# Kernel tuning notes

Hardware: AMD Instinct MI355X
Metric: run time of the kernel (lower is better)

The kernel has to match this reference:

```python
import jax, jax.numpy as jnp
import numpy as np

# Static config matching init_kwargs / input_specs
B, C, H, W, T = 2, 128, 32, 32, 32
OUT = 256
WS, SHIFT, HEADS = 4, 2, 8
MLP = 4 * C
N = WS ** 3          # tokens per 4x4x4 window = 64
D_BLOCKS = 4         # depth=2 -> 2 (no-shift, shift) pairs


def _rel_idx():
    coords = np.stack(np.meshgrid(np.arange(WS), np.arange(WS), np.arange(WS), indexing='ij')).reshape(3, -1)
    rel = (coords[:, :, None] - coords[:, None, :]).transpose(1, 2, 0) + (WS - 1)
    return (rel[..., 0] * (2 * WS - 1) ** 2 + rel[..., 1] * (2 * WS - 1) + rel[..., 2]).astype(np.int32)

REL_IDX = jnp.asarray(_rel_idx())  # [N, N]


def _attn_mask():
    # Faithful port of Block.createmask (H,W,T already multiples of WS)
    img = np.zeros((H, W, T))
    sl = (slice(0, -WS), slice(-WS, -SHIFT), slice(-SHIFT, None))
    cnt = 0
    for hs in sl:
        for ws_ in sl:
            for ts in sl:
                img[hs, ws_, ts] = cnt
                cnt += 1
    m = img.reshape(H // WS, WS, W // WS, WS, T // WS, WS).transpose(0, 2, 4, 1, 3, 5).reshape(-1, N)
    am = m[:, None, :] - m[:, :, None]
    return jnp.asarray(np.where(am != 0, -100.0, 0.0).astype(np.float32))  # [nW, N, N]

MASK = _attn_mask()


def _partition(x):  # [b,H,W,T,c] -> [b*nW, N, c]
    b, c = x.shape[0], x.shape[-1]
    x = x.reshape(b, H // WS, WS, W // WS, WS, T // WS, WS, c).transpose(0, 1, 3, 5, 2, 4, 6, 7)
    return x.reshape(-1, N, c)


def _reverse(wins, b, c):  # [b*nW, N, c] -> [b,H,W,T,c]
    x = wins.reshape(b, H // WS, W // WS, T // WS, WS, WS, WS, c).transpose(0, 1, 4, 2, 5, 3, 6, 7)
    return x.reshape(b, H, W, T, c)


def _ln(x, g, b):
    mu = x.mean(-1, keepdims=True)
    var = ((x - mu) ** 2).mean(-1, keepdims=True)
    return (x - mu) / jnp.sqrt(var + 1e-5) * g + b


def _swin(x, shift, g1, b1, qw, qb, pw, pb, rpb, g2, b2, f1w, f1b, f2w, f2b):
    b, L, c = x.shape
    hd = c // HEADS
    scale = hd ** -0.5
    h = _ln(x, g1, b1).reshape(b, H, W, T, c)
    if shift:
        h = jnp.roll(h, (-SHIFT, -SHIFT, -SHIFT), axis=(1, 2, 3))
    win = _partition(h)  # [b*nW, N, c]
    qkv = (win @ qw.T + qb).reshape(-1, N, 3, HEADS, hd).transpose(2, 0, 3, 1, 4)
    q, k, v = qkv[0] * scale, qkv[1], qkv[2]
    attn = jnp.einsum('bhnd,bhmd->bhnm', q, k) + rpb[REL_IDX].transpose(2, 0, 1)[None]
    if shift:
        nW = MASK.shape[0]
        attn = (attn.reshape(b, nW, HEADS, N, N) + MASK[None, :, None]).reshape(-1, HEADS, N, N)
    attn = jax.nn.softmax(attn, axis=-1)
    o = jnp.einsum('bhnm,bhmd->bhnd', attn, v).transpose(0, 2, 1, 3).reshape(-1, N, c)
    o = o @ pw.T + pb
    h = _reverse(o, b, c)
    if shift:
        h = jnp.roll(h, (SHIFT, SHIFT, SHIFT), axis=(1, 2, 3))
    x = x + h.reshape(b, L, c)
    m = jax.nn.gelu(_ln(x, g2, b2) @ f1w.T + f1b, approximate=False)
    return x + (m @ f2w.T + f2b)


def setup_inputs() -> dict:
    key = jax.random.key(0)
    ks = jax.random.split(key, 10)
    r = lambda i, sh, s=0.02: jax.random.normal(ks[i], sh, jnp.float32) * s
    Dn = D_BLOCKS
    return {
        'x': jax.random.normal(ks[0], (B, C, H, W, T), jnp.float32),
        'norm1_g': jnp.ones((Dn, C), jnp.float32), 'norm1_b': jnp.zeros((Dn, C), jnp.float32),
        'qkv_w': r(1, (Dn, 3 * C, C)), 'qkv_b': jnp.zeros((Dn, 3 * C), jnp.float32),
        'proj_w': r(2, (Dn, C, C)), 'proj_b': jnp.zeros((Dn, C), jnp.float32),
        'rpb': r(3, (Dn, (2 * WS - 1) ** 3, HEADS)),
        'norm2_g': jnp.ones((Dn, C), jnp.float32), 'norm2_b': jnp.zeros((Dn, C), jnp.float32),
        'fc1_w': r(4, (Dn, MLP, C)), 'fc1_b': jnp.zeros((Dn, MLP), jnp.float32),
        'fc2_w': r(5, (Dn, C, MLP)), 'fc2_b': jnp.zeros((Dn, C), jnp.float32),
        'dw_w': r(6, (C, 1, 3, 3, 3), 0.1), 'dw_b': jnp.zeros((C,), jnp.float32),
        'pw_w': r(7, (OUT, C, 1, 1, 1), 0.05), 'pw_b': jnp.zeros((OUT,), jnp.float32),
        'bn_g': jnp.ones((OUT,), jnp.float32), 'bn_b': jnp.zeros((OUT,), jnp.float32),
    }


def reference(x, norm1_g, norm1_b, qkv_w, qkv_b, proj_w, proj_b, rpb, norm2_g, norm2_b,
              fc1_w, fc1_b, fc2_w, fc2_b, dw_w, dw_b, pw_w, pw_b, bn_g, bn_b):
    b = x.shape[0]
    t = x.transpose(0, 2, 3, 4, 1).reshape(b, H * W * T, C)  # b (h w t) c
    shifts = [0, SHIFT, 0, SHIFT]
    for i, s in enumerate(shifts):
        t = _swin(t, s, norm1_g[i], norm1_b[i], qkv_w[i], qkv_b[i], proj_w[i], proj_b[i],
                  rpb[i], norm2_g[i], norm2_b[i], fc1_w[i], fc1_b[i], fc2_w[i], fc2_b[i])
    y = t.reshape(b, H, W, T, C).transpose(0, 4, 1, 2, 3)
    # connectBlock: depthwise 3x3x3 conv + pointwise 1x1x1 conv + BatchNorm3d + ReLU
    dn = ('NCDHW', 'OIDHW', 'NCDHW')
    y = jax.lax.conv_general_dilated(y, dw_w, (1, 1, 1), 'SAME', dimension_numbers=dn,
                                     feature_group_count=C) + dw_b[None, :, None, None, None]
    y = jax.lax.conv_general_dilated(y, pw_w, (1, 1, 1), 'SAME', dimension_numbers=dn) + pw_b[None, :, None, None, None]
    mu = y.mean((0, 2, 3, 4), keepdims=True)
    var = ((y - mu) ** 2).mean((0, 2, 3, 4), keepdims=True)
    y = (y - mu) / jnp.sqrt(var + 1e-5) * bn_g[None, :, None, None, None] + bn_b[None, :, None, None, None]
    return jax.nn.relu(y)
```

## Files before the change

kernel.cpp:

```cpp
#include <hip/hip_runtime.h>
#include <hip/hip_bf16.h>
#include <cstddef>
#include <cstdint>

typedef __attribute__((ext_vector_type(8))) short short8;
typedef __attribute__((ext_vector_type(4))) short short4v;
typedef __attribute__((ext_vector_type(4))) float floatx4;
typedef __hip_bfloat16 bf16;

#define HEADS 8
#define TOK   65536
#define OUTC  256

__device__ inline float b2f(short s) {
    union { unsigned u; float f; } x;
    x.u = ((unsigned)(unsigned short)s) << 16;
    return x.f;
}

__device__ inline floatx4 mfma16(short4v a, short4v b, floatx4 c) {
#if __has_builtin(__builtin_amdgcn_mfma_f32_16x16x16bf16_1k)
    return __builtin_amdgcn_mfma_f32_16x16x16bf16_1k(a, b, c, 0, 0, 0);
#else
    floatx4 d;
    asm volatile("v_mfma_f32_16x16x16_bf16 %0, %1, %2, %3\n\ts_nop 7"
                 : "=v"(d) : "v"(a), "v"(b), "v"(c));
    return d;
#endif
}

__global__ __launch_bounds__(256) void transpose_in_kernel(
    const float* __restrict__ x, float* __restrict__ out, float* __restrict__ tstats)
{
    __shared__ float tile[128 * 65];
    int chunk = blockIdx.x;
    int tid = threadIdx.x;
    int b = chunk >> 9;
    int sp0 = (chunk & 511) * 64;
    #pragma unroll
    for (int l = 0; l < 32; ++l) {
        int idx = l * 256 + tid;
        int c = idx >> 6;
        int s = idx & 63;
        tile[c * 65 + s] = x[(((size_t)(b * 128 + c)) << 15) + sp0 + s];
    }
    __syncthreads();
    #pragma unroll
    for (int l = 0; l < 32; ++l) {
        int idx = l * 256 + tid;
        int s = idx >> 7;
        int c = idx & 127;
        out[((size_t)((b << 15) + sp0 + s)) * 128 + c] = tile[c * 65 + s];
    }
    int s = tid >> 2, q = tid & 3;
    float sm = 0.f, sq = 0.f;
    #pragma unroll
    for (int cc = 0; cc < 32; ++cc) {
        float v = tile[(q * 32 + cc) * 65 + s];
        sm += v; sq += v * v;
    }
    sm += __shfl_xor(sm, 1); sq += __shfl_xor(sq, 1);
    sm += __shfl_xor(sm, 2); sq += __shfl_xor(sq, 2);
    if (q == 0) {
        float mu = sm * (1.0f / 128.0f);
        float var = sq * (1.0f / 128.0f) - mu * mu;
        size_t tok = (size_t)(b << 15) + sp0 + s;
        tstats[tok * 2]     = mu;
        tstats[tok * 2 + 1] = rsqrtf(var + 1e-5f);
    }
}

__global__ __launch_bounds__(256) void prep_kernel(
    const float* __restrict__ qkv_w, const float* __restrict__ proj_w,
    const float* __restrict__ fc1_w, const float* __restrict__ fc2_w,
    const float* __restrict__ pw_w, const float* __restrict__ dw_w,
    bf16* __restrict__ wbf, float* __restrict__ dwt, float* __restrict__ stats)
{
    int i = blockIdx.x * 256 + threadIdx.x;
    float v;
    if (i < 196608)       v = qkv_w[i];
    else if (i < 262144)  v = proj_w[i - 196608];
    else if (i < 524288)  v = fc1_w[i - 262144];
    else if (i < 786432)  v = fc2_w[i - 524288];
    else                  v = pw_w[i - 786432];
    wbf[i] = __float2bfloat16(v);
    if (i < 3456) {
        int c = i / 27, k = i % 27;
        dwt[k * 128 + c] = dw_w[i];
    }
    if (i < 512) stats[i] = 0.f;
}

__global__ __launch_bounds__(256) void pack_kernel(
    const float* __restrict__ fc1_w, const float* __restrict__ fc2_w,
    bf16* __restrict__ pw1, bf16* __restrict__ pw2)
{
    int t = blockIdx.x * 256 + threadIdx.x;
    int i = t >> 17;
    int rem = t & 131071;
    int type = rem >> 16;
    int idx = rem & 65535;
    int j = idx & 7, lane = (idx >> 3) & 63;
    int ln15 = lane & 15, quad = lane >> 4;
    if (type == 0) {
        int nt = (idx >> 9) & 1, kk = (idx >> 10) & 3, wv = (idx >> 12) & 3, cc = (idx >> 14) & 3;
        int row = cc * 128 + wv * 32 + nt * 16 + ln15;
        int col = kk * 32 + quad * 8 + j;
        pw1[i * 65536 + idx] = __float2bfloat16(fc1_w[(size_t)i * 65536 + row * 128 + col]);
    } else {
        int nt = (idx >> 9) & 1, ks = (idx >> 10) & 3, cc = (idx >> 12) & 3, wv = (idx >> 14) & 3;
        int row = wv * 32 + nt * 16 + ln15;
        int col = cc * 128 + ks * 32 + quad * 8 + j;
        pw2[i * 65536 + idx] = __float2bfloat16(fc2_w[(size_t)i * 65536 + row * 512 + col]);
    }
}

__global__ __launch_bounds__(256) void rpe_expand_kernel(
    const float* __restrict__ rpb, float* __restrict__ rpe, int layer)
{
    int t = blockIdx.x * 256 + threadIdx.x;
    int j = t & 63, i = (t >> 6) & 63, head = (t >> 12) & 7, wt = t >> 15;
    int ih = i >> 4, iw = (i >> 2) & 3, it = i & 3;
    int jh = j >> 4, jw = (j >> 2) & 3, jt = j & 3;
    int ridx = ((ih - jh + 3) * 7 + (iw - jw + 3)) * 7 + (it - jt + 3);
    float v = rpb[layer * 2744 + ridx * 8 + head];
    if (wt) {
        bool ok = true;
        if (wt & 4) ok = ok && ((ih >= 2) == (jh >= 2));
        if (wt & 2) ok = ok && ((iw >= 2) == (jw >= 2));
        if (wt & 1) ok = ok && ((it >= 2) == (jt >= 2));
        if (!ok) v -= 100.f;
    }
    rpe[t] = v;
}

__global__ __launch_bounds__(256) void gemm_bf16_kernel(
    const bf16* __restrict__ A, const bf16* __restrict__ Bw,
    const float* __restrict__ bias, bf16* __restrict__ Cb, float* __restrict__ Cf,
    float* __restrict__ aux, const float* __restrict__ p1, const float* __restrict__ p2,
    int M, int N, int K, int mode, int shift)
{
    __shared__ __align__(16) char smem[34816];
    __shared__ float cs[128];
    __shared__ float cq[128];
    short* As = (short*)smem;
    short* Bs = (short*)(smem + 8192);
    int tid = threadIdx.x;
    int lane = tid & 63, wv = tid >> 6;
    int wm = wv >> 1, wn = wv & 1;
    int ln15 = lane & 15, quad = lane >> 4;
    int q8 = quad * 8;
    int nBase = blockIdx.x * 128;
    int mBase = blockIdx.y * 128;
    floatx4 acc[4][4] = {};

    if (mode == 4 && tid < 128) { cs[tid] = 0.f; cq[tid] = 0.f; }

    int srow = tid >> 2, scb = tid & 3;

    int toks[2]; float tmu[2], trs[2];
    if (mode == 0) {
        if (tid < 128) { cs[tid] = p1[tid]; cq[tid] = p2[tid]; }
        #pragma unroll
        for (int i = 0; i < 2; ++i) {
            int m = mBase + srow + i * 64;
            int n = m & 63, w = (m >> 6) & 511, b = m >> 15;
            int ih = n >> 4, iw = (n >> 2) & 3, it = n & 3;
            int wh = w >> 6, ww = (w >> 3) & 7, wt = w & 7;
            int h  = (wh * 4 + ih + shift) & 31;
            int w2 = (ww * 4 + iw + shift) & 31;
            int t  = (wt * 4 + it + shift) & 31;
            toks[i] = (b << 15) + ((h * 32 + w2) * 32 + t);
            tmu[i] = aux[(size_t)toks[i] * 2];
            trs[i] = aux[(size_t)toks[i] * 2 + 1];
        }
        __syncthreads();
    }

    for (int k0 = 0; k0 < K; k0 += 32) {
        if (mode == 0) {
            int cb = k0 + scb * 8;
            #pragma unroll
            for (int i = 0; i < 2; ++i) {
                const float* xr = Cf + (size_t)toks[i] * 128 + cb;
                float4 a0 = *(const float4*)xr;
                float4 a1 = *(const float4*)(xr + 4);
                float mu = tmu[i], rs = trs[i];
                __align__(16) bf16 pk[8];
                pk[0] = __float2bfloat16((a0.x - mu) * rs * cs[cb + 0] + cq[cb + 0]);
                pk[1] = __float2bfloat16((a0.y - mu) * rs * cs[cb + 1] + cq[cb + 1]);
                pk[2] = __float2bfloat16((a0.z - mu) * rs * cs[cb + 2] + cq[cb + 2]);
                pk[3] = __float2bfloat16((a0.w - mu) * rs * cs[cb + 3] + cq[cb + 3]);
                pk[4] = __float2bfloat16((a1.x - mu) * rs * cs[cb + 4] + cq[cb + 4]);
                pk[5] = __float2bfloat16((a1.y - mu) * rs * cs[cb + 5] + cq[cb + 5]);
                pk[6] = __float2bfloat16((a1.z - mu) * rs * cs[cb + 6] + cq[cb + 6]);
                pk[7] = __float2bfloat16((a1.w - mu) * rs * cs[cb + 7] + cq[cb + 7]);
                ((uint4*)As)[i * 256 + tid] = *(const uint4*)pk;
                ((uint4*)Bs)[i * 256 + tid] =
                    *(const uint4*)(Bw + (size_t)(nBase + srow + i * 64) * K + cb);
            }
        } else {
            #pragma unroll
            for (int i = 0; i < 2; ++i) {
                int row = srow + i * 64;
                ((uint4*)As)[i * 256 + tid] =
                    *(const uint4*)(A + (size_t)(mBase + row) * K + k0 + scb * 8);
                ((uint4*)Bs)[i * 256 + tid] =
                    *(const uint4*)(Bw + (size_t)(nBase + row) * K + k0 + scb * 8);
            }
        }
        __syncthreads();
        short8 af[4], bfr[4];
        #pragma unroll
        for (int mt = 0; mt < 4; ++mt)
            af[mt] = *(const short8*)&As[(wm * 64 + mt * 16 + ln15) * 32 + q8];
        #pragma unroll
        for (int nt = 0; nt < 4; ++nt)
            bfr[nt] = *(const short8*)&Bs[(wn * 64 + nt * 16 + ln15) * 32 + q8];
        #pragma unroll
        for (int mt = 0; mt < 4; ++mt)
            #pragma unroll
            for (int nt = 0; nt < 4; ++nt)
                acc[mt][nt] = __builtin_amdgcn_mfma_f32_16x16x32_bf16(
                    af[mt], bfr[nt], acc[mt][nt], 0, 0, 0);
        __syncthreads();
    }

    if (mode == 4) {
        #pragma unroll
        for (int nt = 0; nt < 4; ++nt) {
            int nl = wn * 64 + nt * 16 + ln15;
            float bs = bias[nBase + nl];
            float s = 0.f, sq = 0.f;
            #pragma unroll
            for (int mt = 0; mt < 4; ++mt)
                #pragma unroll
                for (int r = 0; r < 4; ++r) {
                    float v = acc[mt][nt][r] + bs;
                    s += v; sq += v * v;
                }
            atomicAdd(&cs[nl], s);
            atomicAdd(&cq[nl], sq);
        }
        __syncthreads();
        if (tid < 128) {
            atomicAdd(&aux[nBase + tid], cs[tid]);
            atomicAdd(&aux[256 + nBase + tid], cq[tid]);
        }
        return;
    }

    if (mode == 0) {
        bf16* estage = (bf16*)smem;
        float qsc = (nBase == 0) ? 0.25f : 1.0f;
        #pragma unroll
        for (int mt = 0; mt < 4; ++mt)
            #pragma unroll
            for (int nt = 0; nt < 4; ++nt)
                #pragma unroll
                for (int r = 0; r < 4; ++r) {
                    int row = wm * 64 + mt * 16 + quad * 4 + r;
                    int col = wn * 64 + nt * 16 + ln15;
                    estage[row * 136 + col] =
                        __float2bfloat16((acc[mt][nt][r] + bias[nBase + col]) * qsc);
                }
        __syncthreads();
        int row = tid >> 1, hf = tid & 1;
        #pragma unroll
        for (int j = 0; j < 4; ++j) {
            int col = hf * 64 + j * 16;
            *(uint4*)(Cb + (size_t)(mBase + row) * N + nBase + col) =
                *(const uint4*)&estage[row * 136 + col];
            *(uint4*)(Cb + (size_t)(mBase + row) * N + nBase + col + 8) =
                *(const uint4*)&estage[row * 136 + col + 8];
        }
        return;
    }

    if (mode == 2) {
        float* fstage = (float*)smem;
        #pragma unroll
        for (int hf = 0; hf < 2; ++hf) {
            if (wm == hf) {
                #pragma unroll
                for (int mt = 0; mt < 4; ++mt)
                    #pragma unroll
                    for (int nt = 0; nt < 4; ++nt)
                        #pragma unroll
                        for (int r = 0; r < 4; ++r) {
                            int ml = mt * 16 + quad * 4 + r;
                            int col = wn * 64 + nt * 16 + ln15;
                            fstage[ml * 132 + col] = acc[mt][nt][r] + bias[col];
                        }
            }
            __syncthreads();
            int tl = tid >> 2, part = tid & 3;
            int g = mBase + hf * 64 + tl;
            int n_ = g & 63, w = (g >> 6) & 511, b = g >> 15;
            int ih = n_ >> 4, iw = (n_ >> 2) & 3, it = n_ & 3;
            int wh = w >> 6, ww = (w >> 3) & 7, wt = w & 7;
            int h  = (wh * 4 + ih + shift) & 31;
            int w2 = (ww * 4 + iw + shift) & 31;
            int t  = (wt * 4 + it + shift) & 31;
            size_t tok = ((size_t)b << 15) + ((h * 32 + w2) * 32 + t);
            float* dst = aux + tok * 128 + part * 32;
            #pragma unroll
            for (int j = 0; j < 8; ++j) {
                float4 a = *(float4*)(dst + j * 4);
                float4 l = *(const float4*)&fstage[tl * 132 + part * 32 + j * 4];
                a.x += l.x; a.y += l.y; a.z += l.z; a.w += l.w;
                *(float4*)(dst + j * 4) = a;
            }
            __syncthreads();
        }
        return;
    }

    {
        float* fstage = (float*)smem;
        int b = mBase >> 15, sp0 = mBase & 32767;
        #pragma unroll
        for (int hf = 0; hf < 2; ++hf) {
            if (wn == hf) {
                #pragma unroll
                for (int nt = 0; nt < 4; ++nt) {
                    int ncol = nt * 16 + ln15;
                    int nn = nBase + hf * 64 + ncol;
                    float mean = aux[nn] * (1.0f / 65536.0f);
                    float var  = aux[256 + nn] * (1.0f / 65536.0f) - mean * mean;
                    float sc = rsqrtf(var + 1e-5f) * p1[nn];
                    float off = p2[nn] + bias[nn] * sc - mean * sc;
                    #pragma unroll
                    for (int mt = 0; mt < 4; ++mt)
                        #pragma unroll
                        for (int r = 0; r < 4; ++r) {
                            int ml = wm * 64 + mt * 16 + quad * 4 + r;
                            float y = acc[mt][nt][r] * sc + off;
                            fstage[ncol * 132 + ml] = fmaxf(y, 0.f);
                        }
                }
            }
            __syncthreads();
            int nl = tid >> 2, part = tid & 3;
            int nn = nBase + hf * 64 + nl;
            float* dst = Cf + (((size_t)(b * 256 + nn)) << 15) + sp0 + part * 32;
            #pragma unroll
            for (int j = 0; j < 8; ++j)
                *(float4*)(dst + j * 4) = *(const float4*)&fstage[nl * 132 + part * 32 + j * 4];
            __syncthreads();
        }
    }
}

__global__ __launch_bounds__(256, 4) void mlp_kernel(
    float* __restrict__ xbuf, const float* __restrict__ g, const float* __restrict__ bta,
    const bf16* __restrict__ pw1, const float* __restrict__ b1,
    const bf16* __restrict__ pw2, const float* __restrict__ b2,
    bf16* __restrict__ xout16, float* __restrict__ tstats)
{
    __shared__ __align__(16) bf16 smem[64 * 136 * 2];
    bf16* aln  = smem;
    bf16* hidc = smem + 64 * 136;
    float* ostage = (float*)smem;
    int tid = threadIdx.x;
    int lane = tid & 63, wv = tid >> 6;
    int ln15 = lane & 15, quad = lane >> 4;
    int q8 = quad * 8;
    size_t tok0 = (size_t)blockIdx.x * 64;

    #pragma unroll
    for (int itk = 0; itk < 16; ++itk) {
        int t = wv * 16 + itk;
        const float* xp = xbuf + (tok0 + t) * 128;
        float v0 = xp[lane], v1 = xp[lane + 64];
        float s = v0 + v1, sq = v0 * v0 + v1 * v1;
        #pragma unroll
        for (int o = 32; o > 0; o >>= 1) { s += __shfl_xor(s, o); sq += __shfl_xor(sq, o); }
        float mu  = s * (1.0f / 128.0f);
        float var = sq * (1.0f / 128.0f) - mu * mu;
        float rs  = rsqrtf(var + 1e-5f);
        aln[t * 136 + lane]      = __float2bfloat16((v0 - mu) * rs * g[lane]      + bta[lane]);
        aln[t * 136 + lane + 64] = __float2bfloat16((v1 - mu) * rs * g[lane + 64] + bta[lane + 64]);
    }
    __syncthreads();

    floatx4 acc2[4][2] = {};
    #pragma unroll
    for (int cc = 0; cc < 4; ++cc) {
        floatx4 acc[4][2] = {};
        const bf16* p1w = pw1 + (size_t)(cc * 4 + wv) * 4096;
        #pragma unroll
        for (int kk = 0; kk < 4; ++kk) {
            short8 af[4], bfr[2];
            #pragma unroll
            for (int mt = 0; mt < 4; ++mt)
                af[mt] = *(const short8*)&aln[(mt * 16 + ln15) * 136 + kk * 32 + q8];
            #pragma unroll
            for (int nt = 0; nt < 2; ++nt)
                bfr[nt] = *(const short8*)(p1w + kk * 1024 + nt * 512 + lane * 8);
            #pragma unroll
            for (int mt = 0; mt < 4; ++mt)
                #pragma unroll
                for (int nt = 0; nt < 2; ++nt)
                    acc[mt][nt] = __builtin_amdgcn_mfma_f32_16x16x32_bf16(
                        af[mt], bfr[nt], acc[mt][nt], 0, 0, 0);
        }
        if (cc) __syncthreads();
        #pragma unroll
        for (int mt = 0; mt < 4; ++mt)
            #pragma unroll
            for (int nt = 0; nt < 2; ++nt)
                #pragma unroll
                for (int r = 0; r < 4; ++r) {
                    int m = mt * 16 + quad * 4 + r;
                    int ncl = wv * 32 + nt * 16 + ln15;
                    float v = acc[mt][nt][r] + b1[cc * 128 + ncl];
                    float u = v * (0.7978845608f + 0.0356774081f * v * v);
                    v = v * __builtin_amdgcn_rcpf(1.f + __expf(-2.f * u));
                    hidc[m * 136 + ncl] = __float2bfloat16(v);
                }
        __syncthreads();
        const bf16* p2w = pw2 + (size_t)(wv * 4 + cc) * 4096;
        #pragma unroll
        for (int ks = 0; ks < 4; ++ks) {
            short8 af[4], bfr[2];
            #pragma unroll
            for (int mt = 0; mt < 4; ++mt)
                af[mt] = *(const short8*)&hidc[(mt * 16 + ln15) * 136 + ks * 32 + q8];
            #pragma unroll
            for (int nt = 0; nt < 2; ++nt)
                bfr[nt] = *(const short8*)(p2w + ks * 1024 + nt * 512 + lane * 8);
            #pragma unroll
            for (int mt = 0; mt < 4; ++mt)
                #pragma unroll
                for (int nt = 0; nt < 2; ++nt)
                    acc2[mt][nt] = __builtin_amdgcn_mfma_f32_16x16x32_bf16(
                        af[mt], bfr[nt], acc2[mt][nt], 0, 0, 0);
        }
    }
    __syncthreads();

    #pragma unroll
    for (int mt = 0; mt < 4; ++mt)
        #pragma unroll
        for (int nt = 0; nt < 2; ++nt)
            #pragma unroll
            for (int r = 0; r < 4; ++r) {
                int m = mt * 16 + quad * 4 + r;
                int n = wv * 32 + nt * 16 + ln15;
                ostage[m * 132 + n] = acc2[mt][nt][r] + b2[n];
            }
    __syncthreads();

    #pragma unroll
    for (int jj = 0; jj < 8; ++jj) {
        int idx = (jj * 256 + tid) * 4;
        int t = idx >> 7, c = idx & 127;
        float4 v = *(const float4*)(xbuf + tok0 * 128 + idx);
        float4 o = *(const float4*)&ostage[t * 132 + c];
        v.x += o.x; v.y += o.y; v.z += o.z; v.w += o.w;
        *(float4*)(xbuf + tok0 * 128 + idx) = v;
        if (xout16) {
            __align__(8) bf16 hh[4];
            hh[0] = __float2bfloat16(v.x); hh[1] = __float2bfloat16(v.y);
            hh[2] = __float2bfloat16(v.z); hh[3] = __float2bfloat16(v.w);
            *(uint2*)(xout16 + tok0 * 128 + idx) = *(const uint2*)hh;
        }
        float ps = v.x + v.y + v.z + v.w;
        float pq = v.x * v.x + v.y * v.y + v.z * v.z + v.w * v.w;
        #pragma unroll
        for (int o2 = 16; o2 > 0; o2 >>= 1) {
            ps += __shfl_xor(ps, o2); pq += __shfl_xor(pq, o2);
        }
        if ((tid & 31) == 0) {
            float mu = ps * (1.0f / 128.0f);
            float var = pq * (1.0f / 128.0f) - mu * mu;
            size_t tok = tok0 + t;
            tstats[tok * 2]     = mu;
            tstats[tok * 2 + 1] = rsqrtf(var + 1e-5f);
        }
    }
}

__global__ __launch_bounds__(256, 3) void attn_mfma_kernel(
    const bf16* __restrict__ qkv, const float* __restrict__ rpe,
    bf16* __restrict__ outp, int shift)
{
    __shared__ __align__(16) short qs[64 * 392];
    int tid = threadIdx.x;
    int lane = tid & 63, wv = tid >> 6;
    int ln15 = lane & 15, quad = lane >> 4;
    int win = blockIdx.x;
    size_t tok0 = (size_t)win * 64;

    const short* gq = (const short*)qkv + tok0 * 384;
    #pragma unroll
    for (int l = 0; l < 12; ++l) {
        int idx = l * 256 + tid;
        int r = idx / 48, c = idx - r * 48;
        *(uint4*)&qs[r * 392 + c * 8] = *(const uint4*)&gq[r * 384 + c * 8];
    }
    int w = win & 511;
    int wtype = 0;
    if (shift)
        wtype = (((w >> 6) == 7) << 2) | ((((w >> 3) & 7) == 7) << 1) | (int)((w & 7) == 7);
    const float* rpw = rpe + ((size_t)(wtype * 8) << 12);
    __syncthreads();

    floatx4 oacc[2][4];
    #pragma unroll
    for (int hh = 0; hh < 2; ++hh) {
        int head = wv * 2 + hh;
        const float* rph = rpw + ((size_t)head << 12);

        floatx4 acc[4][4];
        #pragma unroll
        for (int jt = 0; jt < 4; ++jt)
            #pragma unroll
            for (int it = 0; it < 4; ++it)
                acc[jt][it] = *(const floatx4*)&rph[(it * 16 + ln15) * 64 + jt * 16 + quad * 4];

        short4v qf[4], kf[4];
        #pragma unroll
        for (int it = 0; it < 4; ++it)
            qf[it] = *(const short4v*)&qs[(it * 16 + ln15) * 392 + head * 16 + quad * 4];
        #pragma unroll
        for (int jt = 0; jt < 4; ++jt)
            kf[jt] = *(const short4v*)&qs[(jt * 16 + ln15) * 392 + 128 + head * 16 + quad * 4];

        #pragma unroll
        for (int jt = 0; jt < 4; ++jt)
            #pragma unroll
            for (int it = 0; it < 4; ++it)
                acc[jt][it] = mfma16(kf[jt], qf[it], acc[jt][it]);

        short4v pf[4][4];
        #pragma unroll
        for (int it = 0; it < 4; ++it) {
            float m = -1e30f;
            #pragma unroll
            for (int jt = 0; jt < 4; ++jt)
                #pragma unroll
                for (int r = 0; r < 4; ++r) m = fmaxf(m, acc[jt][it][r]);
            m = fmaxf(m, __shfl_xor(m, 16));
            m = fmaxf(m, __shfl_xor(m, 32));
            float s = 0.f;
            #pragma unroll
            for (int jt = 0; jt < 4; ++jt)
                #pragma unroll
                for (int r = 0; r < 4; ++r) {
                    float e = __expf(acc[jt][it][r] - m);
                    acc[jt][it][r] = e; s += e;
                }
            s += __shfl_xor(s, 16);
            s += __shfl_xor(s, 32);
            float inv = 1.0f / s;
            #pragma unroll
            for (int jt = 0; jt < 4; ++jt) {
                __align__(8) bf16 pb[4];
                #pragma unroll
                for (int r = 0; r < 4; ++r)
                    pb[r] = __float2bfloat16(acc[jt][it][r] * inv);
                pf[jt][it] = *(const short4v*)pb;
            }
        }

        short4v vf[4];
        #pragma unroll
        for (int jt = 0; jt < 4; ++jt)
            #pragma unroll
            for (int jj = 0; jj < 4; ++jj)
                vf[jt][jj] = qs[(jt * 16 + quad * 4 + jj) * 392 + 256 + head * 16 + ln15];

        #pragma unroll
        for (int it = 0; it < 4; ++it) {
            floatx4 o = {0.f, 0.f, 0.f, 0.f};
            #pragma unroll
            for (int jt = 0; jt < 4; ++jt)
                o = mfma16(vf[jt], pf[jt][it], o);
            oacc[hh][it] = o;
        }
    }
    __syncthreads();

    short* ob = qs;
    #pragma unroll
    for (int hh = 0; hh < 2; ++hh)
        #pragma unroll
        for (int it = 0; it < 4; ++it) {
            __align__(8) bf16 t4[4];
            #pragma unroll
            for (int r = 0; r < 4; ++r) t4[r] = __float2bfloat16(oacc[hh][it][r]);
            *(short4v*)&ob[(it * 16 + ln15) * 136 + (wv * 2 + hh) * 16 + quad * 4] =
                *(const short4v*)t4;
        }
    __syncthreads();

    short* po = (short*)outp + tok0 * 128;
    #pragma unroll
    for (int l = 0; l < 4; ++l) {
        int idx = l * 256 + tid;
        int r = idx >> 4, c = idx & 15;
        *(uint4*)&po[r * 128 + c * 8] = *(const uint4*)&ob[r * 136 + c * 8];
    }
}

__global__ __launch_bounds__(256) void dwconv_kernel(
    const bf16* __restrict__ x, const float* __restrict__ dwt,
    const float* __restrict__ bias, bf16* __restrict__ out)
{
    int blk = blockIdx.x;
    int b = blk >> 9;
    int h = (blk >> 4) & 31;
    int w = ((blk & 15) << 1) | (threadIdx.x >> 7);
    int tid = threadIdx.x & 127;
    int c0 = (tid & 31) * 4;
    int t0 = (tid >> 5) * 8;

    float4 acc[8];
    float4 bs = *(const float4*)&bias[c0];
    #pragma unroll
    for (int o = 0; o < 8; ++o) acc[o] = bs;

    #pragma unroll
    for (int kh = 0; kh < 3; ++kh) {
        int hh = h + kh - 1;
        if (hh < 0 || hh > 31) continue;
        #pragma unroll
        for (int kw = 0; kw < 3; ++kw) {
            int ww = w + kw - 1;
            if (ww < 0 || ww > 31) continue;
            const short* px = (const short*)x +
                ((size_t)(b << 15) + (hh * 32 + ww) * 32) * 128 + c0;
            float4 v[10];
            #pragma unroll
            for (int u = 0; u < 10; ++u) {
                int tt = t0 - 1 + u;
                if (tt >= 0 && tt < 32) {
                    short4v s4 = *(const short4v*)(px + (size_t)tt * 128);
                    v[u].x = b2f(s4[0]); v[u].y = b2f(s4[1]);
                    v[u].z = b2f(s4[2]); v[u].w = b2f(s4[3]);
                } else {
                    v[u].x = v[u].y = v[u].z = v[u].w = 0.f;
                }
            }
            int kb = kh * 9 + kw * 3;
            float4 w0 = *(const float4*)&dwt[(kb + 0) * 128 + c0];
            float4 w1 = *(const float4*)&dwt[(kb + 1) * 128 + c0];
            float4 w2 = *(const float4*)&dwt[(kb + 2) * 128 + c0];
            #pragma unroll
            for (int o = 0; o < 8; ++o) {
                acc[o].x += v[o].x * w0.x + v[o + 1].x * w1.x + v[o + 2].x * w2.x;
                acc[o].y += v[o].y * w0.y + v[o + 1].y * w1.y + v[o + 2].y * w2.y;
                acc[o].z += v[o].z * w0.z + v[o + 1].z * w1.z + v[o + 2].z * w2.z;
                acc[o].w += v[o].w * w0.w + v[o + 1].w * w1.w + v[o + 2].w * w2.w;
            }
        }
    }
    short* po = (short*)out + ((size_t)(b << 15) + (h * 32 + w) * 32 + t0) * 128 + c0;
    #pragma unroll
    for (int o = 0; o < 8; ++o) {
        __align__(8) bf16 h4[4];
        h4[0] = __float2bfloat16(acc[o].x);
        h4[1] = __float2bfloat16(acc[o].y);
        h4[2] = __float2bfloat16(acc[o].z);
        h4[3] = __float2bfloat16(acc[o].w);
        *(uint2*)(po + (size_t)o * 128) = *(const uint2*)h4;
    }
}

extern "C" void kernel_launch(void* const* d_in, const int* in_sizes, int n_in,
                              void* d_out, int out_size, void* d_ws, size_t ws_size,
                              hipStream_t stream)
{
    const float* x_in    = (const float*)d_in[0];
    const float* norm1_g = (const float*)d_in[1];
    const float* norm1_b = (const float*)d_in[2];
    const float* qkv_w   = (const float*)d_in[3];
    const float* qkv_b   = (const float*)d_in[4];
    const float* proj_w  = (const float*)d_in[5];
    const float* proj_b  = (const float*)d_in[6];
    const float* rpb     = (const float*)d_in[7];
    const float* norm2_g = (const float*)d_in[8];
    const float* norm2_b = (const float*)d_in[9];
    const float* fc1_w   = (const float*)d_in[10];
    const float* fc1_b   = (const float*)d_in[11];
    const float* fc2_w   = (const float*)d_in[12];
    const float* fc2_b   = (const float*)d_in[13];
    const float* dw_w    = (const float*)d_in[14];
    const float* dw_b    = (const float*)d_in[15];
    const float* pw_w    = (const float*)d_in[16];
    const float* pw_b    = (const float*)d_in[17];
    const float* bn_g    = (const float*)d_in[18];
    const float* bn_b    = (const float*)d_in[19];
    float* out = (float*)d_out;

    char* ws = (char*)d_ws;
    float* xbuf   = (float*)ws;
    bf16*  wbf    = (bf16*)(ws + 33554432ULL);
    float* dwt    = (float*)(ws + 35651584ULL);
    float* stats  = (float*)(ws + 35717120ULL);
    bf16*  pw1    = (bf16*)(ws + 35782656ULL);
    bf16*  pw2    = (bf16*)(ws + 36306944ULL);
    float* tstats = (float*)(ws + 36831232ULL);
    bf16*  lnbuf  = (bf16*)(ws + 37748736ULL);
    bf16*  attnbuf= (bf16*)(ws + 54525952ULL);
    bf16*  qkvbuf = (bf16*)(ws + 71303168ULL);
    bf16*  dwbuf  = attnbuf;
    bf16*  dcbuf  = lnbuf;
    float* rpe    = (float*)lnbuf;

    bf16* wqkv  = wbf;
    bf16* wproj = wbf + 196608;
    bf16* wpw   = wbf + 786432;

    hipLaunchKernelGGL(prep_kernel, dim3(3200), dim3(256), 0, stream,
                       qkv_w, proj_w, fc1_w, fc2_w, pw_w, dw_w, wbf, dwt, stats);
    hipLaunchKernelGGL(pack_kernel, dim3(2048), dim3(256), 0, stream,
                       fc1_w, fc2_w, pw1, pw2);
    hipLaunchKernelGGL(transpose_in_kernel, dim3(1024), dim3(256), 0, stream,
                       x_in, xbuf, tstats);

    const int shifts[4] = {0, 2, 0, 2};
    for (int i = 0; i < 4; ++i) {
        int s = shifts[i];
        hipLaunchKernelGGL(gemm_bf16_kernel, dim3(3, TOK / 128), dim3(256), 0, stream,
                           (const bf16*)nullptr, wqkv + (size_t)i * 49152, qkv_b + i * 384,
                           qkvbuf, xbuf, tstats,
                           norm1_g + i * 128, norm1_b + i * 128,
                           TOK, 384, 128, 0, s);
        hipLaunchKernelGGL(rpe_expand_kernel, dim3(s ? 1024 : 128), dim3(256), 0, stream,
                           rpb, rpe, i);
        hipLaunchKernelGGL(attn_mfma_kernel, dim3(TOK / 64), dim3(256), 0, stream,
                           qkvbuf, rpe, attnbuf, s);
        hipLaunchKernelGGL(gemm_bf16_kernel, dim3(1, TOK / 128), dim3(256), 0, stream,
                           attnbuf, wproj + (size_t)i * 16384, proj_b + i * 128,
                           (bf16*)nullptr, (float*)nullptr, xbuf,
                           (const float*)nullptr, (const float*)nullptr,
                           TOK, 128, 128, 2, s);
        hipLaunchKernelGGL(mlp_kernel, dim3(TOK / 64), dim3(256), 0, stream,
                           xbuf, norm2_g + i * 128, norm2_b + i * 128,
                           pw1 + (size_t)i * 65536, fc1_b + i * 512,
                           pw2 + (size_t)i * 65536, fc2_b + i * 128,
                           (i == 3) ? dwbuf : (bf16*)nullptr, tstats);
    }

    hipLaunchKernelGGL(dwconv_kernel, dim3(1024), dim3(256), 0, stream,
                       dwbuf, dwt, dw_b, dcbuf);
    hipLaunchKernelGGL(gemm_bf16_kernel, dim3(OUTC / 128, TOK / 128), dim3(256), 0, stream,
                       dcbuf, wpw, pw_b,
                       (bf16*)nullptr, (float*)nullptr, stats,
                       (const float*)nullptr, (const float*)nullptr,
                       TOK, OUTC, 128, 4, 0);
    hipLaunchKernelGGL(gemm_bf16_kernel, dim3(OUTC / 128, TOK / 128), dim3(256), 0, stream,
                       dcbuf, wpw, pw_b,
                       (bf16*)nullptr, out, stats,
                       bn_g, bn_b,
                       TOK, OUTC, 128, 5, 0);
}
```

Measured before the change: 757.9 us.

## Keep MLP hidden activations in registers, chaining fc1 output into fc2 MFMA

The MLP kernel is restructured so each wave owns 16 tokens. fc1 is computed transposed (weights as the A operand), so the GELU output lands in registers already laid out as the A operand of the 16x16x16 fc2 MFMA. This removes the shared-memory round trip and barriers for the hidden tile, and the ostage staging of the output. The weight-packing kernel is changed to match the new fragment order. In exchange, register pressure rises (occupancy hint lowered from 4 to 3 blocks), each wave now streams all weights on its own, and the residual stores become strided scalar writes.

```diff
diff --git a/kernel.cpp b/kernel.cpp
--- a/kernel.cpp
+++ b/kernel.cpp
@@ -100,18 +100,20 @@
     int rem = t & 131071;
     int type = rem >> 16;
     int idx = rem & 65535;
-    int j = idx & 7, lane = (idx >> 3) & 63;
-    int ln15 = lane & 15, quad = lane >> 4;
     if (type == 0) {
-        int nt = (idx >> 9) & 1, kk = (idx >> 10) & 3, wv = (idx >> 12) & 3, cc = (idx >> 14) & 3;
-        int row = cc * 128 + wv * 32 + nt * 16 + ln15;
+        int j = idx & 7, lane = (idx >> 3) & 63;
+        int kk = (idx >> 9) & 3, nt = (idx >> 11) & 15, h = (idx >> 15) & 1;
+        int ln15 = lane & 15, quad = lane >> 4;
+        int row = h * 256 + nt * 16 + ln15;
         int col = kk * 32 + quad * 8 + j;
         pw1[i * 65536 + idx] = __float2bfloat16(fc1_w[(size_t)i * 65536 + row * 128 + col]);
     } else {
-        int nt = (idx >> 9) & 1, ks = (idx >> 10) & 3, cc = (idx >> 12) & 3, wv = (idx >> 14) & 3;
-        int row = wv * 32 + nt * 16 + ln15;
-        int col = cc * 128 + ks * 32 + quad * 8 + j;
-        pw2[i * 65536 + idx] = __float2bfloat16(fc2_w[(size_t)i * 65536 + row * 512 + col]);
+        int j = idx & 3, lane = (idx >> 2) & 63;
+        int ks = (idx >> 8) & 15, ct = (idx >> 12) & 7, h = (idx >> 15) & 1;
+        int ln15 = lane & 15, quad = lane >> 4;
+        int row = ct * 16 + ln15;
+        int k = h * 256 + ks * 16 + quad * 4 + j;
+        pw2[i * 65536 + idx] = __float2bfloat16(fc2_w[(size_t)i * 65536 + row * 512 + k]);
     }
 }
 
@@ -352,16 +354,13 @@
     }
 }
 
-__global__ __launch_bounds__(256, 4) void mlp_kernel(
+__global__ __launch_bounds__(256, 3) void mlp_kernel(
     float* __restrict__ xbuf, const float* __restrict__ g, const float* __restrict__ bta,
     const bf16* __restrict__ pw1, const float* __restrict__ b1,
     const bf16* __restrict__ pw2, const float* __restrict__ b2,
     bf16* __restrict__ xout16, float* __restrict__ tstats)
 {
-    __shared__ __align__(16) bf16 smem[64 * 136 * 2];
-    bf16* aln  = smem;
-    bf16* hidc = smem + 64 * 136;
-    float* ostage = (float*)smem;
+    __shared__ __align__(16) bf16 aln[64 * 136];
     int tid = threadIdx.x;
     int lane = tid & 63, wv = tid >> 6;
     int ln15 = lane & 15, quad = lane >> 4;
@@ -384,100 +383,89 @@
     }
     __syncthreads();
 
-    floatx4 acc2[4][2] = {};
-    #pragma unroll
-    for (int cc = 0; cc < 4; ++cc) {
-        floatx4 acc[4][2] = {};
-        const bf16* p1w = pw1 + (size_t)(cc * 4 + wv) * 4096;
-        #pragma unroll
-        for (int kk = 0; kk < 4; ++kk) {
-            short8 af[4], bfr[2];
-            #pragma unroll
-            for (int mt = 0; mt < 4; ++mt)
-                af[mt] = *(const short8*)&aln[(mt * 16 + ln15) * 136 + kk * 32 + q8];
-            #pragma unroll
-            for (int nt = 0; nt < 2; ++nt)
-                bfr[nt] = *(const short8*)(p1w + kk * 1024 + nt * 512 + lane * 8);
-            #pragma unroll
-            for (int mt = 0; mt < 4; ++mt)
-                #pragma unroll
-                for (int nt = 0; nt < 2; ++nt)
-                    acc[mt][nt] = __builtin_amdgcn_mfma_f32_16x16x32_bf16(
-                        af[mt], bfr[nt], acc[mt][nt], 0, 0, 0);
-        }
-        if (cc) __syncthreads();
-        #pragma unroll
-        for (int mt = 0; mt < 4; ++mt)
-            #pragma unroll
-            for (int nt = 0; nt < 2; ++nt)
-                #pragma unroll
-                for (int r = 0; r < 4; ++r) {
-                    int m = mt * 16 + quad * 4 + r;
-                    int ncl = wv * 32 + nt * 16 + ln15;
-                    float v = acc[mt][nt][r] + b1[cc * 128 + ncl];
-                    float u = v * (0.7978845608f + 0.0356774081f * v * v);
-                    v = v * __builtin_amdgcn_rcpf(1.f + __expf(-2.f * u));
-                    hidc[m * 136 + ncl] = __float2bfloat16(v);
-                }
-        __syncthreads();
-        const bf16* p2w = pw2 + (size_t)(wv * 4 + cc) * 4096;
-        #pragma unroll
-        for (int ks = 0; ks < 4; ++ks) {
-            short8 af[4], bfr[2];
-            #pragma unroll
-            for (int mt = 0; mt < 4; ++mt)
-                af[mt] = *(const short8*)&hidc[(mt * 16 + ln15) * 136 + ks * 32 + q8];
-            #pragma unroll
-            for (int nt = 0; nt < 2; ++nt)
-                bfr[nt] = *(const short8*)(p2w + ks * 1024 + nt * 512 + lane * 8);
-            #pragma unroll
-            for (int mt = 0; mt < 4; ++mt)
-                #pragma unroll
-                for (int nt = 0; nt < 2; ++nt)
-                    acc2[mt][nt] = __builtin_amdgcn_mfma_f32_16x16x32_bf16(
-                        af[mt], bfr[nt], acc2[mt][nt], 0, 0, 0);
-        }
-    }
-    __syncthreads();
-
-    #pragma unroll
-    for (int mt = 0; mt < 4; ++mt)
-        #pragma unroll
-        for (int nt = 0; nt < 2; ++nt)
+    short8 xb[4];
+    #pragma unroll
+    for (int kk = 0; kk < 4; ++kk)
+        xb[kk] = *(const short8*)&aln[(wv * 16 + ln15) * 136 + kk * 32 + q8];
+
+    floatx4 acc2[8] = {};
+
+    #pragma unroll
+    for (int h = 0; h < 2; ++h) {
+        short4v pa[16];
+        #pragma unroll
+        for (int nt = 0; nt < 16; ++nt) {
+            floatx4 ah = {0.f, 0.f, 0.f, 0.f};
+            const bf16* p1w = pw1 + (((h * 16 + nt) * 4) << 9);
+            #pragma unroll
+            for (int kk = 0; kk < 4; ++kk) {
+                short8 w1f = *(const short8*)(p1w + (kk << 9) + lane * 8);
+                ah = __builtin_amdgcn_mfma_f32_16x16x32_bf16(w1f, xb[kk], ah, 0, 0, 0);
+            }
+            float4 bv = *(const float4*)&b1[h * 256 + nt * 16 + quad * 4];
+            __align__(8) bf16 tmp[4];
             #pragma unroll
             for (int r = 0; r < 4; ++r) {
-                int m = mt * 16 + quad * 4 + r;
-                int n = wv * 32 + nt * 16 + ln15;
-                ostage[m * 132 + n] = acc2[mt][nt][r] + b2[n];
-            }
-    __syncthreads();
-
-    #pragma unroll
-    for (int jj = 0; jj < 8; ++jj) {
-        int idx = (jj * 256 + tid) * 4;
-        int t = idx >> 7, c = idx & 127;
-        float4 v = *(const float4*)(xbuf + tok0 * 128 + idx);
-        float4 o = *(const float4*)&ostage[t * 132 + c];
-        v.x += o.x; v.y += o.y; v.z += o.z; v.w += o.w;
-        *(float4*)(xbuf + tok0 * 128 + idx) = v;
-        if (xout16) {
-            __align__(8) bf16 hh[4];
-            hh[0] = __float2bfloat16(v.x); hh[1] = __float2bfloat16(v.y);
-            hh[2] = __float2bfloat16(v.z); hh[3] = __float2bfloat16(v.w);
-            *(uint2*)(xout16 + tok0 * 128 + idx) = *(const uint2*)hh;
-        }
-        float ps = v.x + v.y + v.z + v.w;
-        float pq = v.x * v.x + v.y * v.y + v.z * v.z + v.w * v.w;
-        #pragma unroll
-        for (int o2 = 16; o2 > 0; o2 >>= 1) {
-            ps += __shfl_xor(ps, o2); pq += __shfl_xor(pq, o2);
-        }
-        if ((tid & 31) == 0) {
-            float mu = ps * (1.0f / 128.0f);
-            float var = pq * (1.0f / 128.0f) - mu * mu;
-            size_t tok = tok0 + t;
+                float v = ah[r] + ((const float*)&bv)[r];
+                float u = v * (0.7978845608f + 0.0356774081f * v * v);
+                v = v * __builtin_amdgcn_rcpf(1.f + __expf(-2.f * u));
+                tmp[r] = __float2bfloat16(v);
+            }
+            pa[nt] = *(const short4v*)tmp;
+        }
+        #pragma unroll
+        for (int ct = 0; ct < 8; ++ct) {
+            const bf16* p2w = pw2 + (((h * 8 + ct) * 16) << 8);
+            #pragma unroll
+            for (int ks = 0; ks < 16; ++ks) {
+                short4v w2f = *(const short4v*)(p2w + (ks << 8) + lane * 4);
+                acc2[ct] = mfma16(pa[ks], w2f, acc2[ct]);
+            }
+        }
+    }
+
+    float ps[4] = {}, pq[4] = {};
+    #pragma unroll
+    for (int ct = 0; ct < 8; ++ct) {
+        float b2s = b2[ct * 16 + ln15];
+        #pragma unroll
+        for (int r = 0; r < 4; ++r) {
+            int tl = wv * 16 + quad * 4 + r;
+            float* p = xbuf + (tok0 + tl) * 128 + ct * 16 + ln15;
+            float v = *p + acc2[ct][r] + b2s;
+            *p = v;
+            ps[r] += v; pq[r] += v * v;
+            if (xout16)
+                aln[tl * 136 + ct * 16 + ln15] = __float2bfloat16(v);
+        }
+    }
+    #pragma unroll
+    for (int r = 0; r < 4; ++r) {
+        #pragma unroll
+        for (int o = 8; o > 0; o >>= 1) {
+            ps[r] += __shfl_xor(ps[r], o);
+            pq[r] += __shfl_xor(pq[r], o);
+        }
+    }
+    if (ln15 == 0) {
+        #pragma unroll
+        for (int r = 0; r < 4; ++r) {
+            size_t tok = tok0 + wv * 16 + quad * 4 + r;
+            float mu = ps[r] * (1.0f / 128.0f);
+            float var = pq[r] * (1.0f / 128.0f) - mu * mu;
             tstats[tok * 2]     = mu;
             tstats[tok * 2 + 1] = rsqrtf(var + 1e-5f);
+        }
+    }
+
+    if (xout16) {
+        __syncthreads();
+        short* po = (short*)xout16 + tok0 * 128;
+        #pragma unroll
+        for (int l = 0; l < 4; ++l) {
+            int idx = l * 256 + tid;
+            int r = idx >> 4, c8 = idx & 15;
+            *(uint4*)&po[r * 128 + c8 * 8] = *(const uint4*)&aln[r * 136 + c8 * 8];
         }
     }
 }
```

Result: slower. 890.4 us (+17.5%).
